# Kernel tuning notes

Hardware: AMD Instinct MI355X
Metric: run time of the kernel (lower is better)

## Reference

```python
import jax, jax.numpy as jnp
import numpy as np

EGO_W = 1.85 + 0.5   # ego width + delta
EGO_L = 4.084 + 0.5  # ego length + delta
SOFT_MARGIN = 1.5
WEIGHT = 1.0


def setup_inputs() -> dict:
    key = jax.random.key(0)
    k1, k2, k3, k4 = jax.random.split(key, 4)
    B, T, N = 4096, 12, 512
    pred_abs = jax.random.normal(k1, (B, T, 2), dtype=jnp.float32)
    gt_bboxes = jax.random.normal(k2, (B, N, 9), dtype=jnp.float32)
    gt_ego_fut_masks = jax.random.randint(k3, (B, T), 0, 2, dtype=jnp.int32)
    agent_mask = jax.random.randint(k4, (B, N), 0, 2, dtype=jnp.int32)
    return {
        "pred_abs": pred_abs,
        "gt_bboxes": gt_bboxes,
        "gt_ego_fut_masks": gt_ego_fut_masks,
        "agent_mask": agent_mask,
    }


def reference(pred_abs, gt_bboxes, gt_ego_fut_masks, agent_mask):
    # pred_abs: [B,T,2], gt_bboxes: [B,N,9], masks: [B,T] / [B,N]
    cx = gt_bboxes[:, :, 0]  # [B,N]
    cy = gt_bboxes[:, :, 1]
    ax = gt_bboxes[:, :, 3]
    ay = gt_bboxes[:, :, 4]

    ex = pred_abs[:, :, 0][:, :, None]  # [B,T,1]
    ey = pred_abs[:, :, 1][:, :, None]

    dist_x = jnp.abs(ex - cx[:, None, :])  # [B,T,N]
    dist_y = jnp.abs(ey - cy[:, None, :])

    thresh_x = EGO_W / 2 + ax / 2 + SOFT_MARGIN  # [B,N]
    thresh_y = EGO_L / 2 + ay / 2 + SOFT_MARGIN

    pen_x = jax.nn.relu(thresh_x[:, None, :] - dist_x)
    pen_y = jax.nn.relu(thresh_y[:, None, :] - dist_y)

    ego_valid = (gt_ego_fut_masks >= 1)[:, :, None]     # [B,T,1]
    agent_valid = (agent_mask >= 1)[:, None, :]          # [B,1,N]
    valid = (ego_valid & agent_valid).astype(pen_x.dtype)

    loss = jnp.sum(pen_x * pen_y * valid)

    n_valid = jnp.maximum(jnp.sum(gt_ego_fut_masks >= 1).astype(jnp.float32), 1.0)
    return loss / n_valid * WEIGHT
```

## Files before the change

### kernel.cpp

```cpp
#include <hip/hip_runtime.h>


#define T_DIM 12
#define N_DIM 512
#define SLAB4 1152

__global__ __launch_bounds__(256) void collision_loss_main(
    const float* __restrict__ pred_abs,
    const float* __restrict__ gt_bboxes,
    const int*   __restrict__ ego_masks,
    const int*   __restrict__ agent_mask,
    float2* __restrict__ ws)
{
    __shared__ float4 s_slab4[SLAB4];
    __shared__ float  s_ex[T_DIM];
    __shared__ float  s_ey[T_DIM];
    __shared__ float  s_part[4];

    const int b   = blockIdx.x;
    const int tid = threadIdx.x;

    const float4* __restrict__ src4 =
        (const float4*)(gt_bboxes + (size_t)b * (N_DIM * 9));
    #pragma unroll
    for (int i = 0; i < 4; ++i)
        s_slab4[tid + i * 256] = src4[tid + i * 256];
    if (tid < SLAB4 - 1024)
        s_slab4[tid + 1024] = src4[tid + 1024];

    int ev = 0;
    if (tid < T_DIM) {
        ev = (ego_masks[b * T_DIM + tid] >= 1) ? 1 : 0;
        const float ex = pred_abs[(b * T_DIM + tid) * 2 + 0];
        const float ey = pred_abs[(b * T_DIM + tid) * 2 + 1];
        s_ex[tid] = ev ? ex : 1e30f;
        s_ey[tid] = ev ? ey : 1e30f;
    }
    const unsigned long long bm = __ballot(ev != 0);
    const int cnt = __popcll(bm);

    const int av0 = agent_mask[b * N_DIM + tid] >= 1;
    const int av1 = agent_mask[b * N_DIM + tid + 256] >= 1;

    __syncthreads();

    const float* __restrict__ s_bbox = (const float*)s_slab4;
    const int o0 = tid * 9, o1 = (tid + 256) * 9;
    const float cx0 = s_bbox[o0 + 0], cy0 = s_bbox[o0 + 1];
    const float ax0 = s_bbox[o0 + 3], ay0 = s_bbox[o0 + 4];
    const float cx1 = s_bbox[o1 + 0], cy1 = s_bbox[o1 + 1];
    const float ax1 = s_bbox[o1 + 3], ay1 = s_bbox[o1 + 4];

    const float tx0 = av0 ? ((1.85f + 0.5f) * 0.5f + ax0 * 0.5f + 1.5f) : -1e30f;
    const float tx1 = av1 ? ((1.85f + 0.5f) * 0.5f + ax1 * 0.5f + 1.5f) : -1e30f;
    const float ty0 = (4.084f + 0.5f) * 0.5f + ay0 * 0.5f + 1.5f;
    const float ty1 = (4.084f + 0.5f) * 0.5f + ay1 * 0.5f + 1.5f;

    float acc = 0.0f;
    #pragma unroll
    for (int t = 0; t < T_DIM; ++t) {
        const float ex = s_ex[t], ey = s_ey[t];
        const float px0 = fmaxf(tx0 - fabsf(ex - cx0), 0.0f);
        const float py0 = fmaxf(ty0 - fabsf(ey - cy0), 0.0f);
        const float px1 = fmaxf(tx1 - fabsf(ex - cx1), 0.0f);
        const float py1 = fmaxf(ty1 - fabsf(ey - cy1), 0.0f);
        acc += px0 * py0 + px1 * py1;
    }

    #pragma unroll
    for (int off = 32; off > 0; off >>= 1) acc += __shfl_down(acc, off);
    const int wave = tid >> 6;
    if ((tid & 63) == 0) s_part[wave] = acc;
    __syncthreads();
    if (tid == 0) {
        const float L = s_part[0] + s_part[1] + s_part[2] + s_part[3];
        ws[b] = make_float2(L, (float)cnt);
    }
}

__global__ __launch_bounds__(1024) void collision_loss_reduce(
    const float2* __restrict__ ws, float* __restrict__ out, int nB)
{
    __shared__ float s_l[16];
    __shared__ float s_c[16];
    const int tid = threadIdx.x;

    float l = 0.0f, c = 0.0f;
    for (int i = tid; i < nB; i += 1024) {
        const float2 v = ws[i];
        l += v.x;
        c += v.y;
    }
    #pragma unroll
    for (int off = 32; off > 0; off >>= 1) {
        l += __shfl_down(l, off);
        c += __shfl_down(c, off);
    }
    const int wave = tid >> 6;
    if ((tid & 63) == 0) { s_l[wave] = l; s_c[wave] = c; }
    __syncthreads();
    if (tid == 0) {
        float L = 0.0f, C = 0.0f;
        #pragma unroll
        for (int w = 0; w < 16; ++w) { L += s_l[w]; C += s_c[w]; }
        out[0] = L / fmaxf(C, 1.0f);
    }
}

extern "C" void kernel_launch(void* const* d_in, const int* in_sizes, int n_in,
                              void* d_out, int out_size, void* d_ws, size_t ws_size,
                              hipStream_t stream)
{
    const float* pred_abs   = (const float*)d_in[0];
    const float* gt_bboxes  = (const float*)d_in[1];
    const int*   ego_masks  = (const int*)d_in[2];
    const int*   agent_mask = (const int*)d_in[3];
    float* out = (float*)d_out;

    const int B = in_sizes[0] / (T_DIM * 2);

    float2* ws = (float2*)d_ws;

    collision_loss_main<<<dim3(B), 256, 0, stream>>>(
        pred_abs, gt_bboxes, ego_masks, agent_mask, ws);

    collision_loss_reduce<<<dim3(1), 1024, 0, stream>>>(ws, out, B);
}
```

Before: 22.78 us.

## Process two batches per block and load bboxes directly from global memory

Each block now handles two batch rows, halving the grid, and the bbox fields are read straight into registers with an unaligned float4 load plus a scalar load instead of staging the whole 9-float slab through LDS. This removes the LDS copy and the strided LDS reads, and gives each thread four agents. The trade-offs are misaligned float4 accesses (stride 36 bytes), uncoalesced global reads that touch only 5 of the 9 fields per agent, and the assumption that B is even.

```diff
diff --git a/kernel.cpp b/kernel.cpp
--- a/kernel.cpp
+++ b/kernel.cpp
@@ -3,7 +3,6 @@
 
 #define T_DIM 12
 #define N_DIM 512
-#define SLAB4 1152
 
 __global__ __launch_bounds__(256) void collision_loss_main(
     const float* __restrict__ pred_abs,
@@ -12,59 +11,68 @@
     const int*   __restrict__ agent_mask,
     float2* __restrict__ ws)
 {
-    __shared__ float4 s_slab4[SLAB4];
-    __shared__ float  s_ex[T_DIM];
-    __shared__ float  s_ey[T_DIM];
-    __shared__ float  s_part[4];
+    __shared__ float s_ex[2][T_DIM];
+    __shared__ float s_ey[2][T_DIM];
+    __shared__ float s_part[4];
 
-    const int b   = blockIdx.x;
+    const int b0  = blockIdx.x * 2;
     const int tid = threadIdx.x;
 
-    const float4* __restrict__ src4 =
-        (const float4*)(gt_bboxes + (size_t)b * (N_DIM * 9));
-    #pragma unroll
-    for (int i = 0; i < 4; ++i)
-        s_slab4[tid + i * 256] = src4[tid + i * 256];
-    if (tid < SLAB4 - 1024)
-        s_slab4[tid + 1024] = src4[tid + 1024];
-
     int ev = 0;
-    if (tid < T_DIM) {
-        ev = (ego_masks[b * T_DIM + tid] >= 1) ? 1 : 0;
-        const float ex = pred_abs[(b * T_DIM + tid) * 2 + 0];
-        const float ey = pred_abs[(b * T_DIM + tid) * 2 + 1];
-        s_ex[tid] = ev ? ex : 1e30f;
-        s_ey[tid] = ev ? ey : 1e30f;
+    if (tid < 2 * T_DIM) {
+        const int bb = tid / T_DIM;
+        const int t  = tid % T_DIM;
+        const int b  = b0 + bb;
+        ev = (ego_masks[b * T_DIM + t] >= 1) ? 1 : 0;
+        const float ex = pred_abs[(b * T_DIM + t) * 2 + 0];
+        const float ey = pred_abs[(b * T_DIM + t) * 2 + 1];
+        s_ex[bb][t] = ev ? ex : 1e30f;
+        s_ey[bb][t] = ev ? ey : 1e30f;
     }
     const unsigned long long bm = __ballot(ev != 0);
     const int cnt = __popcll(bm);
 
-    const int av0 = agent_mask[b * N_DIM + tid] >= 1;
-    const int av1 = agent_mask[b * N_DIM + tid + 256] >= 1;
+    const float* base = gt_bboxes + (size_t)b0 * (N_DIM * 9);
+    const float4 f0 = *(const float4*)(base + (size_t)(tid      ) * 9);
+    const float  g0 = *(base + (size_t)(tid      ) * 9 + 4);
+    const float4 f1 = *(const float4*)(base + (size_t)(tid + 256) * 9);
+    const float  g1 = *(base + (size_t)(tid + 256) * 9 + 4);
+    const float4 f2 = *(const float4*)(base + (size_t)(tid + 512) * 9);
+    const float  g2 = *(base + (size_t)(tid + 512) * 9 + 4);
+    const float4 f3 = *(const float4*)(base + (size_t)(tid + 768) * 9);
+    const float  g3 = *(base + (size_t)(tid + 768) * 9 + 4);
+
+    const int* am = agent_mask + b0 * N_DIM;
+    const int av0 = am[tid]       >= 1;
+    const int av1 = am[tid + 256] >= 1;
+    const int av2 = am[tid + 512] >= 1;
+    const int av3 = am[tid + 768] >= 1;
+
+    const float tx0 = av0 ? (1.175f + f0.w * 0.5f + 1.5f) : -1e30f;
+    const float tx1 = av1 ? (1.175f + f1.w * 0.5f + 1.5f) : -1e30f;
+    const float tx2 = av2 ? (1.175f + f2.w * 0.5f + 1.5f) : -1e30f;
+    const float tx3 = av3 ? (1.175f + f3.w * 0.5f + 1.5f) : -1e30f;
+    const float ty0 = 2.292f + g0 * 0.5f + 1.5f;
+    const float ty1 = 2.292f + g1 * 0.5f + 1.5f;
+    const float ty2 = 2.292f + g2 * 0.5f + 1.5f;
+    const float ty3 = 2.292f + g3 * 0.5f + 1.5f;
 
     __syncthreads();
-
-    const float* __restrict__ s_bbox = (const float*)s_slab4;
-    const int o0 = tid * 9, o1 = (tid + 256) * 9;
-    const float cx0 = s_bbox[o0 + 0], cy0 = s_bbox[o0 + 1];
-    const float ax0 = s_bbox[o0 + 3], ay0 = s_bbox[o0 + 4];
-    const float cx1 = s_bbox[o1 + 0], cy1 = s_bbox[o1 + 1];
-    const float ax1 = s_bbox[o1 + 3], ay1 = s_bbox[o1 + 4];
-
-    const float tx0 = av0 ? ((1.85f + 0.5f) * 0.5f + ax0 * 0.5f + 1.5f) : -1e30f;
-    const float tx1 = av1 ? ((1.85f + 0.5f) * 0.5f + ax1 * 0.5f + 1.5f) : -1e30f;
-    const float ty0 = (4.084f + 0.5f) * 0.5f + ay0 * 0.5f + 1.5f;
-    const float ty1 = (4.084f + 0.5f) * 0.5f + ay1 * 0.5f + 1.5f;
 
     float acc = 0.0f;
     #pragma unroll
     for (int t = 0; t < T_DIM; ++t) {
-        const float ex = s_ex[t], ey = s_ey[t];
-        const float px0 = fmaxf(tx0 - fabsf(ex - cx0), 0.0f);
-        const float py0 = fmaxf(ty0 - fabsf(ey - cy0), 0.0f);
-        const float px1 = fmaxf(tx1 - fabsf(ex - cx1), 0.0f);
-        const float py1 = fmaxf(ty1 - fabsf(ey - cy1), 0.0f);
-        acc += px0 * py0 + px1 * py1;
+        const float exA = s_ex[0][t], eyA = s_ey[0][t];
+        const float exB = s_ex[1][t], eyB = s_ey[1][t];
+        const float px0 = fmaxf(tx0 - fabsf(exA - f0.x), 0.0f);
+        const float py0 = fmaxf(ty0 - fabsf(eyA - f0.y), 0.0f);
+        const float px1 = fmaxf(tx1 - fabsf(exA - f1.x), 0.0f);
+        const float py1 = fmaxf(ty1 - fabsf(eyA - f1.y), 0.0f);
+        const float px2 = fmaxf(tx2 - fabsf(exB - f2.x), 0.0f);
+        const float py2 = fmaxf(ty2 - fabsf(eyB - f2.y), 0.0f);
+        const float px3 = fmaxf(tx3 - fabsf(exB - f3.x), 0.0f);
+        const float py3 = fmaxf(ty3 - fabsf(eyB - f3.y), 0.0f);
+        acc += px0 * py0 + px1 * py1 + px2 * py2 + px3 * py3;
     }
 
     #pragma unroll
@@ -74,19 +82,19 @@
     __syncthreads();
     if (tid == 0) {
         const float L = s_part[0] + s_part[1] + s_part[2] + s_part[3];
-        ws[b] = make_float2(L, (float)cnt);
+        ws[blockIdx.x] = make_float2(L, (float)cnt);
     }
 }
 
 __global__ __launch_bounds__(1024) void collision_loss_reduce(
-    const float2* __restrict__ ws, float* __restrict__ out, int nB)
+    const float2* __restrict__ ws, float* __restrict__ out, int nP)
 {
     __shared__ float s_l[16];
     __shared__ float s_c[16];
     const int tid = threadIdx.x;
 
     float l = 0.0f, c = 0.0f;
-    for (int i = tid; i < nB; i += 1024) {
+    for (int i = tid; i < nP; i += 1024) {
         const float2 v = ws[i];
         l += v.x;
         c += v.y;
@@ -118,11 +126,12 @@
     float* out = (float*)d_out;
 
     const int B = in_sizes[0] / (T_DIM * 2);
+    const int grid = B / 2;
 
     float2* ws = (float2*)d_ws;
 
-    collision_loss_main<<<dim3(B), 256, 0, stream>>>(
+    collision_loss_main<<<dim3(grid), 256, 0, stream>>>(
         pred_abs, gt_bboxes, ego_masks, agent_mask, ws);
 
-    collision_loss_reduce<<<dim3(1), 1024, 0, stream>>>(ws, out, B);
+    collision_loss_reduce<<<dim3(1), 1024, 0, stream>>>(ws, out, grid);
 }
```

After: 21.02 us. -7.7%, faster.
